# Optimization experiments

Hardware: AMD Instinct MI355X
Metric: run time of the kernel (lower is better)

The kernel has to match this reference:

```python
import jax, jax.numpy as jnp
import numpy as np

B, L, G, HID, H, D = 2, 4096, 256, 768, 12, 64
R = 127            # local_radius
BLK = R + 1        # block_len = 128
N = L // BLK       # 32 blocks (L divisible by BLK)
W = 2 * R + 1      # 255 local window
V = 32             # relative vocab size


def setup_inputs() -> dict:
    ks = jax.random.split(jax.random.key(0), 40)
    inp = {}
    inp["long_input"] = jax.random.normal(ks[0], (B, L, HID), jnp.float32)
    inp["global_input"] = jax.random.normal(ks[1], (B, G, HID), jnp.float32)
    inp["l2l_att_mask"] = jax.random.randint(ks[2], (B, L, W), 0, 2, jnp.int32)
    inp["g2g_att_mask"] = jax.random.randint(ks[3], (B, G, G), 0, 2, jnp.int32)
    inp["l2g_att_mask"] = jax.random.randint(ks[4], (B, L, G), 0, 2, jnp.int32)
    inp["g2l_att_mask"] = jax.random.randint(ks[5], (B, G, L), 0, 2, jnp.int32)
    inp["l2l_relative_att_ids"] = jax.random.randint(ks[6], (B, L, W), 0, V, jnp.int32)
    inp["g2g_relative_att_ids"] = jax.random.randint(ks[7], (B, G, G), 0, V, jnp.int32)
    inp["l2g_relative_att_ids"] = jax.random.randint(ks[8], (B, L, G), 0, V, jnp.int32)
    inp["g2l_relative_att_ids"] = jax.random.randint(ks[9], (B, G, L), 0, V, jnp.int32)
    i = 10
    for nm in ["q_long", "k_long", "v_long", "q_glob", "k_glob", "v_glob"]:
        inp["w" + nm] = 0.02 * jax.random.normal(ks[i], (HID, H * D), jnp.float32); i += 1
        inp["b" + nm] = jnp.zeros((H * D,), jnp.float32)
    inp["rel_emb_long"] = 0.5 * jax.random.normal(ks[i], (V, H, D), jnp.float32); i += 1
    inp["rel_bias_long"] = jnp.zeros((V, H), jnp.float32)
    inp["rel_emb_glob"] = 0.5 * jax.random.normal(ks[i], (V, H, D), jnp.float32); i += 1
    inp["rel_bias_glob"] = jnp.zeros((V, H), jnp.float32)
    inp["wo_long"] = 0.02 * jax.random.normal(ks[i], (H * D, HID), jnp.float32); i += 1
    inp["bo_long"] = jnp.zeros((HID,), jnp.float32)
    inp["wo_glob"] = 0.02 * jax.random.normal(ks[i], (H * D, HID), jnp.float32); i += 1
    inp["bo_glob"] = jnp.zeros((HID,), jnp.float32)
    return inp


def _expand_local(x):
    """[B, L, W] local-window ids -> blocked [B, N, BLK, 3*BLK] (skew + pad),
    zeroing entries outside the local window or outside the sequence."""
    xb = x.reshape(B, N, BLK, W)
    p = jnp.arange(BLK)[:, None]        # query pos within block
    c = jnp.arange(3 * BLK)[None, :]    # key pos within 3-block window
    r = c - p - 1                       # index into the 2R+1 window
    valid = (r >= 0) & (r < W)
    rc = jnp.clip(r, 0, W - 1)
    out = jnp.take_along_axis(xb, jnp.broadcast_to(rc, (B, N, BLK, 3 * BLK)), axis=-1)
    j = (jnp.arange(N)[:, None, None] - 1) * BLK + c  # absolute key position
    valid_full = valid[None] & (j >= 0) & (j < L)     # [N, BLK, 3*BLK]
    return out * valid_full[None].astype(x.dtype)


def reference(long_input, global_input,
              l2l_att_mask, g2g_att_mask, l2g_att_mask, g2l_att_mask,
              l2l_relative_att_ids, g2g_relative_att_ids,
              l2g_relative_att_ids, g2l_relative_att_ids,
              wq_long, bq_long, wk_long, bk_long, wv_long, bv_long,
              wq_glob, bq_glob, wk_glob, bk_glob, wv_glob, bv_glob,
              rel_emb_long, rel_bias_long, rel_emb_glob, rel_bias_glob,
              wo_long, bo_long, wo_glob, bo_glob):
    scale = 1.0 / jnp.sqrt(jnp.float32(D))

    def proj(x, w, b):
        return (x @ w + b).reshape(x.shape[0], x.shape[1], H, D)

    lq, lk, lv = proj(long_input, wq_long, bq_long), proj(long_input, wk_long, bk_long), proj(long_input, wv_long, bv_long)
    gq, gk, gv = proj(global_input, wq_glob, bq_glob), proj(global_input, wk_glob, bk_glob), proj(global_input, wv_glob, bv_glob)

    # ---- long tokens: blocked local attention fused with side (global) keys ----
    qb = lq.reshape(B, N, BLK, H, D)

    def concat3(x):
        xb = x.reshape(B, N, BLK, H, D)
        pad = jnp.zeros_like(xb[:, :1])
        xp = jnp.concatenate([pad, xb, pad], axis=1)  # [B, N+2, BLK, H, D]
        return jnp.concatenate([xp[:, :-2], xp[:, 1:-1], xp[:, 2:]], axis=2)  # [B,N,3BLK,H,D]

    keys = jnp.concatenate([concat3(lk), jnp.broadcast_to(gk[:, None], (B, N, G, H, D))], axis=2)
    vals = jnp.concatenate([concat3(lv), jnp.broadcast_to(gv[:, None], (B, N, G, H, D))], axis=2)

    mask = jnp.concatenate([_expand_local(l2l_att_mask), l2g_att_mask.reshape(B, N, BLK, G)], axis=-1)
    ids = jnp.concatenate([_expand_local(l2l_relative_att_ids), l2g_relative_att_ids.reshape(B, N, BLK, G)], axis=-1)

    scores = jnp.einsum('bnqhd,bnkhd->bnqkh', qb, keys)
    rel_all = jnp.einsum('bnqhd,rhd->bnqrh', qb, rel_emb_long) + rel_bias_long
    rel = jnp.take_along_axis(rel_all, jnp.broadcast_to(ids[..., None], ids.shape + (H,)), axis=3)
    scores = (scores + rel) * scale
    scores = scores - 10000.0 * (1.0 - mask[..., None].astype(scores.dtype))
    probs = jax.nn.softmax(scores, axis=3)
    long_ctx = jnp.einsum('bnqkh,bnkhd->bnqhd', probs, vals).reshape(B, L, H * D)
    long_out = long_ctx @ wo_long + bo_long

    # ---- global tokens: full attention over [global; long] keys ----
    kf = jnp.concatenate([gk, lk], axis=1)
    vf = jnp.concatenate([gv, lv], axis=1)
    gmask = jnp.concatenate([g2g_att_mask, g2l_att_mask], axis=-1)
    gids = jnp.concatenate([g2g_relative_att_ids, g2l_relative_att_ids], axis=-1)
    gs = jnp.einsum('bqhd,bkhd->bqkh', gq, kf)
    grel_all = jnp.einsum('bqhd,rhd->bqrh', gq, rel_emb_glob) + rel_bias_glob
    grel = jnp.take_along_axis(grel_all, jnp.broadcast_to(gids[..., None], gids.shape + (H,)), axis=2)
    gs = (gs + grel) * scale
    gs = gs - 10000.0 * (1.0 - gmask[..., None].astype(gs.dtype))
    gp = jax.nn.softmax(gs, axis=2)
    glob_ctx = jnp.einsum('bqkh,bkhd->bqhd', gp, vf).reshape(B, G, H * D)
    glob_out = glob_ctx @ wo_glob + bo_glob

    return long_out, glob_out
```

## Files before the change

kernel.cpp:

```cpp
#include <hip/hip_runtime.h>
#include <hip/hip_bf16.h>

typedef unsigned short u16;
typedef unsigned char u8;
typedef __attribute__((ext_vector_type(8))) short bf16x8;
typedef __attribute__((ext_vector_type(4))) float f32x4;

#define BB 2
#define LL 4096
#define GG 256
#define HH 12
#define DD 64
#define NB 32
#define WW 255
#define VV 32
#define NCHUNK 17
#define LKEY 640
#define GKEY 4352
#define WMAT 589824

__device__ __forceinline__ float bf2f(u16 u) {
  return __uint_as_float(((unsigned)u) << 16);
}
__device__ __forceinline__ u16 f2bf(float f) {
  unsigned u = __float_as_uint(f);
  u += 0x7FFFu + ((u >> 16) & 1u);
  return (u16)(u >> 16);
}
__device__ __forceinline__ float4 ld4bf(const u16* p) {
  ushort4 q = *reinterpret_cast<const ushort4*>(p);
  return make_float4(bf2f(q.x), bf2f(q.y), bf2f(q.z), bf2f(q.w));
}
__device__ __forceinline__ float ldx1(const void* p, size_t idx, bool f32m) {
  if (f32m) return reinterpret_cast<const float*>(p)[idx];
  return bf2f(reinterpret_cast<const u16*>(p)[idx]);
}
__device__ __forceinline__ void gload16(const u16* src, u16* ldsdst) {
  __builtin_amdgcn_global_load_lds(
      (const __attribute__((address_space(1))) unsigned int*)src,
      (__attribute__((address_space(3))) unsigned int*)ldsdst, 16, 0, 0);
}

__global__ void detect_dtype(const void* __restrict__ x, int* __restrict__ flag) {
  __shared__ int cnt;
  if (threadIdx.x == 0) cnt = 0;
  __syncthreads();
  const u16* p = reinterpret_cast<const u16*>(x);
  int c = 0;
  for (int i = threadIdx.x; i < 4096; i += 256) {
    int e = (p[i] >> 7) & 0xFF;
    if (e >= 134) c++;
  }
  atomicAdd(&cnt, c);
  __syncthreads();
  if (threadIdx.x == 0) *flag = (cnt >= 64) ? 1 : 0;
}

__global__ __launch_bounds__(256)
void pack_l(const int* __restrict__ m_l2l, const int* __restrict__ m_l2g,
            const int* __restrict__ i_l2l, const int* __restrict__ i_l2g,
            u8* __restrict__ pk) {
  const unsigned idx = blockIdx.x * 256u + threadIdx.x;
  const unsigned c = idx % (unsigned)LKEY;
  const unsigned bt = idx / (unsigned)LKEY;
  const int t = bt & (LL - 1);
  int mask = 0, id = 0;
  if (c < 384u) {
    const int rr = (int)c - (t & 127) - 1;
    const int jabs = (((t >> 7) - 1) << 7) + (int)c;
    if (rr >= 0 && rr < WW && jabs >= 0 && jabs < LL) {
      const size_t base = (size_t)bt * WW + rr;
      mask = m_l2l[base]; id = i_l2l[base];
    }
  } else {
    const size_t base = (size_t)bt * GG + (c - 384u);
    mask = m_l2g[base]; id = i_l2g[base];
  }
  pk[idx] = (u8)((id & 31) | ((mask ^ 1) << 7));
}

__global__ __launch_bounds__(256)
void pack_g(const int* __restrict__ m_g2g, const int* __restrict__ m_g2l,
            const int* __restrict__ i_g2g, const int* __restrict__ i_g2l,
            u8* __restrict__ pk) {
  const unsigned idx = blockIdx.x * 256u + threadIdx.x;
  const unsigned c = idx % (unsigned)GKEY;
  const unsigned bq = idx / (unsigned)GKEY;
  int mask, id;
  if (c < 256u) {
    const size_t base = (size_t)bq * GG + c;
    mask = m_g2g[base]; id = i_g2g[base];
  } else {
    const size_t base = (size_t)bq * (size_t)LL + (c - 256u);
    mask = m_g2l[base]; id = i_g2l[base];
  }
  pk[idx] = (u8)((id & 31) | ((mask ^ 1) << 7));
}

__global__ __launch_bounds__(256)
void wprep(const void* __restrict__ W0, const void* __restrict__ W1,
           const void* __restrict__ W2, const void* __restrict__ W3,
           const void* __restrict__ W4, const void* __restrict__ W5,
           u16* __restrict__ wt, const int* __restrict__ flagp) {
  const bool f32m = (*flagp != 0);
  const int mat = blockIdx.z;
  const void* Wm = (mat == 0) ? W0 : (mat == 1) ? W1 : (mat == 2) ? W2
                   : (mat == 3) ? W3 : (mat == 4) ? W4 : W5;
  const int n0 = blockIdx.x << 6, k0 = blockIdx.y << 6;
  const int tid = threadIdx.x;
  __shared__ u16 T[64][72];
  {
    const int r = tid >> 2, c0 = (tid & 3) << 4;
    if (f32m) {
      const float* wp = reinterpret_cast<const float*>(Wm) + (size_t)(k0 + r) * 768 + n0 + c0;
      #pragma unroll
      for (int j = 0; j < 16; j += 4) {
        float4 v = *reinterpret_cast<const float4*>(wp + j);
        T[r][c0 + j + 0] = f2bf(v.x); T[r][c0 + j + 1] = f2bf(v.y);
        T[r][c0 + j + 2] = f2bf(v.z); T[r][c0 + j + 3] = f2bf(v.w);
      }
    } else {
      const u16* wp = reinterpret_cast<const u16*>(Wm) + (size_t)(k0 + r) * 768 + n0 + c0;
      *reinterpret_cast<int4*>(&T[r][c0]) = reinterpret_cast<const int4*>(wp)[0];
      *reinterpret_cast<int4*>(&T[r][c0 + 8]) = reinterpret_cast<const int4*>(wp)[1];
    }
  }
  __syncthreads();
  {
    const int n = tid >> 2, kc0 = (tid & 3) << 4;
    u16 buf[16];
    #pragma unroll
    for (int j = 0; j < 16; j++) buf[j] = T[kc0 + j][n];
    u16* op = wt + ((size_t)mat * WMAT) + (size_t)(n0 + n) * 768 + k0 + kc0;
    *reinterpret_cast<int4*>(op) = *reinterpret_cast<int4*>(buf);
    *reinterpret_cast<int4*>(op + 8) = *reinterpret_cast<int4*>(buf + 8);
  }
}

__global__ __launch_bounds__(256)
void xprep(const void* __restrict__ x, u16* __restrict__ out,
           const int* __restrict__ flagp) {
  const bool f32m = (*flagp != 0);
  const size_t i = ((size_t)blockIdx.x * 256 + threadIdx.x) << 3;
  if (f32m) {
    const float* p = reinterpret_cast<const float*>(x) + i;
    float4 a = *reinterpret_cast<const float4*>(p);
    float4 b = *reinterpret_cast<const float4*>(p + 4);
    u16 o[8] = {f2bf(a.x), f2bf(a.y), f2bf(a.z), f2bf(a.w),
                f2bf(b.x), f2bf(b.y), f2bf(b.z), f2bf(b.w)};
    *reinterpret_cast<int4*>(out + i) = *reinterpret_cast<int4*>(o);
  } else {
    *reinterpret_cast<int4*>(out + i) =
        *reinterpret_cast<const int4*>(reinterpret_cast<const u16*>(x) + i);
  }
}

#define GEMM_CORE(A_, Wt_, row0_, ncol0_)                                        \
  __shared__ u16 lds[16384];                                                     \
  const int tid = threadIdx.x;                                                   \
  const int w = tid >> 6, l = tid & 63;                                          \
  const int lm = l & 15, quad = l >> 4;                                          \
  const int wr = w >> 1, wc = w & 1;                                             \
  const int rb = (w << 5) + (l >> 3);                                            \
  const int c8 = (l & 7) ^ (l >> 3);                                             \
  const u16* asrc = A_ + (size_t)(row0_ + rb) * 768 + (c8 << 3);                 \
  const u16* bsrc = Wt_ + (size_t)(ncol0_ + rb) * 768 + (c8 << 3);               \
  u16* adst = lds + (w << 11) + (l << 3);                                        \
  u16* bdst = adst + 8192;                                                       \
  f32x4 acc[4][4];                                                               \
  _Pragma("unroll")                                                              \
  for (int mt = 0; mt < 4; mt++)                                                 \
    _Pragma("unroll")                                                            \
    for (int nt = 0; nt < 4; nt++) acc[mt][nt] = (f32x4){0.f, 0.f, 0.f, 0.f};    \
  const char* abase = reinterpret_cast<const char*>(lds);                        \
  const char* bbase = abase + 16384;                                             \
  const int xorv = (lm & 7) << 4;                                                \
  for (int k0 = 0; k0 < 768; k0 += 64) {                                         \
    __syncthreads();                                                             \
    _Pragma("unroll")                                                            \
    for (int i = 0; i < 4; i++) gload16(asrc + k0 + i * 6144, adst + (i << 9));  \
    _Pragma("unroll")                                                            \
    for (int i = 0; i < 4; i++) gload16(bsrc + k0 + i * 6144, bdst + (i << 9));  \
    __syncthreads();                                                             \
    _Pragma("unroll")                                                            \
    for (int kk = 0; kk < 2; kk++) {                                             \
      bf16x8 af[4], bfr[4];                                                      \
      _Pragma("unroll")                                                          \
      for (int mt = 0; mt < 4; mt++)                                             \
        af[mt] = *reinterpret_cast<const bf16x8*>(                               \
            abase + ((wr << 6) + (mt << 4) + lm) * 128 +                         \
            (((kk << 6) + (quad << 4)) ^ xorv));                                 \
      _Pragma("unroll")                                                          \
      for (int nt = 0; nt < 4; nt++)                                             \
        bfr[nt] = *reinterpret_cast<const bf16x8*>(                              \
            bbase + ((wc << 6) + (nt << 4) + lm) * 128 +                         \
            (((kk << 6) + (quad << 4)) ^ xorv));                                 \
      _Pragma("unroll")                                                          \
      for (int mt = 0; mt < 4; mt++)                                             \
        _Pragma("unroll")                                                        \
        for (int nt = 0; nt < 4; nt++)                                           \
          acc[mt][nt] = __builtin_amdgcn_mfma_f32_16x16x32_bf16(                 \
              af[mt], bfr[nt], acc[mt][nt], 0, 0, 0);                            \
    }                                                                            \
  }

__global__ __launch_bounds__(256)
void gemm_qkv(const u16* __restrict__ A, const u16* __restrict__ Wt,
              const void* __restrict__ b0, const void* __restrict__ b1,
              const void* __restrict__ b2,
              u16* __restrict__ C0, u16* __restrict__ C1, u16* __restrict__ C2,
              const int* __restrict__ flagp) {
  const bool f32m = (*flagp != 0);
  int lx = blockIdx.x, ly = blockIdx.y;
  if (gridDim.y == 64) {
    const int fid = blockIdx.x + gridDim.x * blockIdx.y;
    const int x = fid & 7, r = fid >> 3;
    ly = (x << 3) | (r & 7);
    lx = r >> 3;
  }
  const int row0 = ly << 7;
  const int ncol0 = lx << 7;
  GEMM_CORE(A, Wt, row0, ncol0)

  const int which = lx / 6;
  const void* bias = (which == 0) ? b0 : ((which == 1) ? b1 : b2);
  u16* Cv = (which == 0) ? C0 : ((which == 1) ? C1 : C2);
  const float sc = (which == 0) ? 0.125f : 1.0f;
  const int colw = (lx % 6) << 7;
  #pragma unroll
  for (int nt = 0; nt < 4; nt++) {
    const int gcol = colw + (wc << 6) + (nt << 4) + lm;
    const float bv = ldx1(bias, gcol, f32m);
    #pragma unroll
    for (int mt = 0; mt < 4; mt++)
      #pragma unroll
      for (int r = 0; r < 4; r++) {
        const int grow = row0 + (wr << 6) + (mt << 4) + (quad << 2) + r;
        Cv[(size_t)grow * 768 + gcol] = f2bf((acc[mt][nt][r] + bv) * sc);
      }
  }
}

__global__ __launch_bounds__(256)
void gemm_out(const u16* __restrict__ A, const u16* __restrict__ Wt,
              const void* __restrict__ bias, void* __restrict__ Cv,
              size_t c_off, const int* __restrict__ flagp) {
  const bool f32m = (*flagp != 0);
  int lx = blockIdx.x, ly = blockIdx.y;
  if (gridDim.y == 64) {
    const int fid = blockIdx.x + gridDim.x * blockIdx.y;
    const int x = fid & 7, r = fid >> 3;
    ly = (x << 3) | (r & 7);
    lx = r >> 3;
  }
  const int row0 = ly << 7;
  const int ncol0 = lx << 7;
  GEMM_CORE(A, Wt, row0, ncol0)

  #pragma unroll
  for (int nt = 0; nt < 4; nt++) {
    const int gcol = ncol0 + (wc << 6) + (nt << 4) + lm;
    const float bv = ldx1(bias, gcol, f32m);
    #pragma unroll
    for (int mt = 0; mt < 4; mt++)
      #pragma unroll
      for (int r = 0; r < 4; r++) {
        const int grow = row0 + (wr << 6) + (mt << 4) + (quad << 2) + r;
        const float v = acc[mt][nt][r] + bv;
        if (f32m)
          reinterpret_cast<float*>(Cv)[c_off + (size_t)grow * 768 + gcol] = v;
        else
          reinterpret_cast<u16*>(Cv)[c_off + (size_t)grow * 768 + gcol] = f2bf(v);
      }
  }
}

__global__ __launch_bounds__(256)
void relk(const u16* __restrict__ Q, const void* __restrict__ emb,
          const void* __restrict__ bias, u16* __restrict__ outp, int T,
          const int* __restrict__ flagp) {
  const bool f32m = (*flagp != 0);
  const int h = blockIdx.y, b = blockIdx.z;
  const int t0 = blockIdx.x << 6;
  const int tid = threadIdx.x;
  __shared__ float Qst[64][68];
  __shared__ float Es[64][36];
  #pragma unroll
  for (int i = 0; i < 4; i++) {
    const int idx = tid + (i << 8);
    const int tt = idx >> 4, d = (idx & 15) << 2;
    float4 v = ld4bf(Q + (((size_t)b * T + t0 + tt) * HH + h) * DD + d);
    Qst[d + 0][tt] = v.x; Qst[d + 1][tt] = v.y;
    Qst[d + 2][tt] = v.z; Qst[d + 3][tt] = v.w;
  }
  #pragma unroll
  for (int i = 0; i < 8; i++) {
    const int idx = tid + (i << 8);
    const int r = idx >> 6, d = idx & 63;
    Es[d][r] = ldx1(emb, ((size_t)r * HH + h) * DD + d, f32m);
  }
  __syncthreads();
  const int tq = (tid & 31) << 1;
  const int r0 = (tid >> 5) << 2;
  float acc[2][4] = {};
  #pragma unroll 8
  for (int d = 0; d < 64; d++) {
    float2 qq = *reinterpret_cast<const float2*>(&Qst[d][tq]);
    float4 e = *reinterpret_cast<const float4*>(&Es[d][r0]);
    acc[0][0] += qq.x * e.x; acc[0][1] += qq.x * e.y;
    acc[0][2] += qq.x * e.z; acc[0][3] += qq.x * e.w;
    acc[1][0] += qq.y * e.x; acc[1][1] += qq.y * e.y;
    acc[1][2] += qq.y * e.z; acc[1][3] += qq.y * e.w;
  }
  float bv[4];
  #pragma unroll
  for (int j = 0; j < 4; j++) bv[j] = ldx1(bias, (size_t)(r0 + j) * HH + h, f32m) * 0.125f;
  #pragma unroll
  for (int i = 0; i < 2; i++) {
    ushort4 o;
    o.x = f2bf(acc[i][0] + bv[0]); o.y = f2bf(acc[i][1] + bv[1]);
    o.z = f2bf(acc[i][2] + bv[2]); o.w = f2bf(acc[i][3] + bv[3]);
    *reinterpret_cast<ushort4*>(&outp[(((size_t)b * T + t0 + tq + i) * HH + h) * VV + r0]) = o;
  }
}

__global__ __launch_bounds__(512)
void lattn(const u16* __restrict__ lq, const u16* __restrict__ lk, const u16* __restrict__ lv,
           const u16* __restrict__ gk, const u16* __restrict__ gv,
           const u8* __restrict__ pkl, const u16* __restrict__ rel,
           u16* __restrict__ lctx) {
  const int fid = blockIdx.x + 12 * (blockIdx.y + (blockIdx.z << 5));
  const int hg = fid >> 3;
  const int h = hg % 12;
  const int fl = (fid & 7) + ((hg / 12) << 3);
  const int n = fl & 31, b = fl >> 5;
  const int tid = threadIdx.x;
  __shared__ u16 Kt[64][72];
  __shared__ u16 Vt[64][74];
  __shared__ u16 Pt[128][74];
  __shared__ u16 Rl[128][36];

  const int lane = tid & 63, wv = tid >> 6;
  const int ln = lane & 15, quad = lane >> 4;
  const int tbase = n << 7;

  {
    const int qr = (wv << 4) + (lane >> 2);
    const int seg = (lane & 3) << 3;
    *reinterpret_cast<int4*>(&Rl[qr][seg]) = *reinterpret_cast<const int4*>(
        rel + (((size_t)b * LL + tbase + qr) * HH + h) * VV + seg);
  }

  bf16x8 aq[2];
  {
    const int t = tbase + (wv << 4) + ln;
    const u16* qp = lq + (((size_t)b * LL + t) * HH + h) * DD + (quad << 3);
    aq[0] = *reinterpret_cast<const bf16x8*>(qp);
    aq[1] = *reinterpret_cast<const bf16x8*>(qp + 32);
  }

  const u8* pkb = pkl + ((size_t)b * LL + tbase) * LKEY;
  const int skey = tid >> 3, sdg = (tid & 7) << 3;

  f32x4 Oacc[4];
  #pragma unroll
  for (int dt = 0; dt < 4; dt++) Oacc[dt] = (f32x4){0.f, 0.f, 0.f, 0.f};
  float lpart[4] = {};

  for (int tile = 0; tile < 10; tile++) {
    const int c0 = tile << 6;
    const bool isg = (tile >= 6);

    float badd[16];
    #pragma unroll
    for (int r = 0; r < 4; r++) {
      const int qrow = (wv << 4) + (quad << 2) + r;
      const u8* prow = pkb + qrow * LKEY + c0 + ln;
      #pragma unroll
      for (int kt = 0; kt < 4; kt++) {
        const u8 pb = prow[kt << 4];
        const float rv = bf2f(Rl[qrow][pb & 31]);
        badd[(kt << 2) + r] = (pb & 0x80) ? (rv - 10000.f) : rv;
      }
    }

    __syncthreads();
    {
      int4 kraw = {0, 0, 0, 0}, vraw = {0, 0, 0, 0};
      if (isg) {
        const size_t base = (((size_t)b * GG + (c0 - 384) + skey) * HH + h) * DD + sdg;
        kraw = *reinterpret_cast<const int4*>(gk + base);
        vraw = *reinterpret_cast<const int4*>(gv + base);
      } else {
        const int jabs = ((n - 1) << 7) + c0 + skey;
        if (jabs >= 0 && jabs < LL) {
          const size_t base = (((size_t)b * LL + jabs) * HH + h) * DD + sdg;
          kraw = *reinterpret_cast<const int4*>(lk + base);
          vraw = *reinterpret_cast<const int4*>(lv + base);
        }
      }
      *reinterpret_cast<int4*>(&Kt[skey][sdg]) = kraw;
      u16 vb[8];
      *reinterpret_cast<int4*>(vb) = vraw;
      #pragma unroll
      for (int j = 0; j < 8; j++) Vt[sdg + j][skey] = vb[j];
    }
    __syncthreads();

    f32x4 Sacc[4];
    #pragma unroll
    for (int kt = 0; kt < 4; kt++) Sacc[kt] = (f32x4){0.f, 0.f, 0.f, 0.f};
    __builtin_amdgcn_s_setprio(1);
    #pragma unroll
    for (int kk = 0; kk < 2; kk++) {
      bf16x8 bk[4];
      #pragma unroll
      for (int kt = 0; kt < 4; kt++)
        bk[kt] = *reinterpret_cast<const bf16x8*>(&Kt[(kt << 4) + ln][(kk << 5) + (quad << 3)]);
      #pragma unroll
      for (int kt = 0; kt < 4; kt++)
        Sacc[kt] = __builtin_amdgcn_mfma_f32_16x16x32_bf16(aq[kk], bk[kt], Sacc[kt], 0, 0, 0);
    }
    __builtin_amdgcn_s_setprio(0);

    #pragma unroll
    for (int kt = 0; kt < 4; kt++)
      #pragma unroll
      for (int r = 0; r < 4; r++) {
        const int ql = (wv << 4) + (quad << 2) + r;
        float s = fminf(fmaxf(Sacc[kt][r], -60.f), 60.f) + badd[(kt << 2) + r];
        const u16 p16 = f2bf(__expf(s));
        Pt[ql][(kt << 4) + ln] = p16;
        lpart[r] += bf2f(p16);
      }

    __builtin_amdgcn_s_setprio(1);
    #pragma unroll
    for (int kk = 0; kk < 2; kk++) {
      bf16x8 ap = *reinterpret_cast<const bf16x8*>(&Pt[(wv << 4) + ln][(kk << 5) + (quad << 3)]);
      #pragma unroll
      for (int dt = 0; dt < 4; dt++) {
        bf16x8 bv = *reinterpret_cast<const bf16x8*>(&Vt[(dt << 4) + ln][(kk << 5) + (quad << 3)]);
        Oacc[dt] = __builtin_amdgcn_mfma_f32_16x16x32_bf16(ap, bv, Oacc[dt], 0, 0, 0);
      }
    }
    __builtin_amdgcn_s_setprio(0);
  }

  #pragma unroll
  for (int r = 0; r < 4; r++) {
    float v = lpart[r];
    v += __shfl_xor(v, 1); v += __shfl_xor(v, 2);
    v += __shfl_xor(v, 4); v += __shfl_xor(v, 8);
    const float inv = 1.0f / v;
    const int t = tbase + (wv << 4) + (quad << 2) + r;
    const size_t base = (((size_t)b * LL + t) * HH + h) * DD;
    #pragma unroll
    for (int dt = 0; dt < 4; dt++)
      lctx[base + (dt << 4) + ln] = f2bf(Oacc[dt][r] * inv);
  }
}

__global__ __launch_bounds__(256)
void gattn(const u16* __restrict__ gq, const u16* __restrict__ gk, const u16* __restrict__ gv,
           const u16* __restrict__ lk, const u16* __restrict__ lv,
           const u8* __restrict__ pkg, const u16* __restrict__ relg,
           float* __restrict__ po, float* __restrict__ pl) {
  const int fid = blockIdx.x + 12 * (blockIdx.y + 17 * blockIdx.z);
  const int hg = fid >> 3;
  const int h = hg % 12;
  const int fl = (fid & 7) + ((hg / 12) << 3);
  const int chunk = fl % 17;
  const int bqt = fl / 17;
  const int b = bqt >> 2, qt = bqt & 3;
  const int tid = threadIdx.x;
  __shared__ u16 Kt[64][72];
  __shared__ u16 Vt[64][74];
  __shared__ u16 Pt[64][74];
  __shared__ u16 Rg[64][36];

  const int lane = tid & 63, wv = tid >> 6;
  const int ln = lane & 15, quad = lane >> 4;
  const int kbase = chunk << 8;
  const bool isgg = (chunk == 0);

  {
    const int qr = (wv << 4) + (lane >> 2);
    const int seg = (lane & 3) << 3;
    *reinterpret_cast<int4*>(&Rg[qr][seg]) = *reinterpret_cast<const int4*>(
        relg + (((size_t)b * GG + (qt << 6) + qr) * HH + h) * VV + seg);
  }

  bf16x8 aq[2];
  {
    const int qa = (qt << 6) + (wv << 4) + ln;
    const u16* qp = gq + (((size_t)b * GG + qa) * HH + h) * DD + (quad << 3);
    aq[0] = *reinterpret_cast<const bf16x8*>(qp);
    aq[1] = *reinterpret_cast<const bf16x8*>(qp + 32);
  }

  const u8* pkb = pkg + ((size_t)b * GG + (qt << 6)) * GKEY;

  f32x4 Oacc[4];
  #pragma unroll
  for (int dt = 0; dt < 4; dt++) Oacc[dt] = (f32x4){0.f, 0.f, 0.f, 0.f};
  float lpart[4] = {};

  for (int tile = 0; tile < 4; tile++) {
    const int c0 = kbase + (tile << 6);

    float badd[16];
    #pragma unroll
    for (int r = 0; r < 4; r++) {
      const int qrow = (wv << 4) + (quad << 2) + r;
      const u8* prow = pkb + qrow * GKEY + c0 + ln;
      #pragma unroll
      for (int kt = 0; kt < 4; kt++) {
        const u8 pb = prow[kt << 4];
        const float rv = bf2f(Rg[qrow][pb & 31]);
        badd[(kt << 2) + r] = (pb & 0x80) ? (rv - 10000.f) : rv;
      }
    }

    __syncthreads();
    #pragma unroll
    for (int p = 0; p < 2; p++) {
      const int idx = tid + (p << 8);
      const int key = idx >> 3, dg = (idx & 7) << 3;
      const int kc = c0 + key;
      int4 kraw, vraw;
      if (isgg) {
        const size_t base = (((size_t)b * GG + kc) * HH + h) * DD + dg;
        kraw = *reinterpret_cast<const int4*>(gk + base);
        vraw = *reinterpret_cast<const int4*>(gv + base);
      } else {
        const size_t base = (((size_t)b * LL + (kc - 256)) * HH + h) * DD + dg;
        kraw = *reinterpret_cast<const int4*>(lk + base);
        vraw = *reinterpret_cast<const int4*>(lv + base);
      }
      *reinterpret_cast<int4*>(&Kt[key][dg]) = kraw;
      u16 vb[8];
      *reinterpret_cast<int4*>(vb) = vraw;
      #pragma unroll
      for (int j = 0; j < 8; j++) Vt[dg + j][key] = vb[j];
    }
    __syncthreads();

    f32x4 Sacc[4];
    #pragma unroll
    for (int kt = 0; kt < 4; kt++) Sacc[kt] = (f32x4){0.f, 0.f, 0.f, 0.f};
    __builtin_amdgcn_s_setprio(1);
    #pragma unroll
    for (int kk = 0; kk < 2; kk++) {
      bf16x8 bk[4];
      #pragma unroll
      for (int kt = 0; kt < 4; kt++)
        bk[kt] = *reinterpret_cast<const bf16x8*>(&Kt[(kt << 4) + ln][(kk << 5) + (quad << 3)]);
      #pragma unroll
      for (int kt = 0; kt < 4; kt++)
        Sacc[kt] = __builtin_amdgcn_mfma_f32_16x16x32_bf16(aq[kk], bk[kt], Sacc[kt], 0, 0, 0);
    }
    __builtin_amdgcn_s_setprio(0);

    #pragma unroll
    for (int kt = 0; kt < 4; kt++)
      #pragma unroll
      for (int r = 0; r < 4; r++) {
        const int ql = (wv << 4) + (quad << 2) + r;
        float s = fminf(fmaxf(Sacc[kt][r], -60.f), 60.f) + badd[(kt << 2) + r];
        const u16 p16 = f2bf(__expf(s));
        Pt[ql][(kt << 4) + ln] = p16;
        lpart[r] += bf2f(p16);
      }

    __builtin_amdgcn_s_setprio(1);
    #pragma unroll
    for (int kk = 0; kk < 2; kk++) {
      bf16x8 ap = *reinterpret_cast<const bf16x8*>(&Pt[(wv << 4) + ln][(kk << 5) + (quad << 3)]);
      #pragma unroll
      for (int dt = 0; dt < 4; dt++) {
        bf16x8 bv = *reinterpret_cast<const bf16x8*>(&Vt[(dt << 4) + ln][(kk << 5) + (quad << 3)]);
        Oacc[dt] = __builtin_amdgcn_mfma_f32_16x16x32_bf16(ap, bv, Oacc[dt], 0, 0, 0);
      }
    }
    __builtin_amdgcn_s_setprio(0);
  }

  #pragma unroll
  for (int r = 0; r < 4; r++) {
    float v = lpart[r];
    v += __shfl_xor(v, 1); v += __shfl_xor(v, 2);
    v += __shfl_xor(v, 4); v += __shfl_xor(v, 8);
    const int qa = (qt << 6) + (wv << 4) + (quad << 2) + r;
    if (ln == 0)
      pl[(((size_t)chunk * BB + b) * HH + h) * GG + qa] = v;
    const size_t base = ((((size_t)chunk * BB + b) * HH + h) * GG + qa) * DD;
    #pragma unroll
    for (int dt = 0; dt < 4; dt++)
      po[base + (dt << 4) + ln] = Oacc[dt][r];
  }
}

__global__ __launch_bounds__(256)
void gcombine(const float* __restrict__ po, const float* __restrict__ pl,
              u16* __restrict__ gctx) {
  const int flat = blockIdx.x * 256 + threadIdx.x;
  const int d = flat & 63;
  const int rest = flat >> 6;
  const int h = rest % HH;
  const int bq = rest / HH;
  const int b = bq >> 8, qg = bq & 255;
  float so = 0.f, sl = 0.f;
  #pragma unroll
  for (int c = 0; c < NCHUNK; c++) {
    so += po[((((size_t)c * BB + b) * HH + h) * GG + qg) * DD + d];
    sl += pl[(((size_t)c * BB + b) * HH + h) * GG + qg];
  }
  gctx[flat] = f2bf(so / sl);
}

extern "C" void kernel_launch(void* const* d_in, const int* in_sizes, int n_in,
                              void* d_out, int out_size, void* d_ws, size_t ws_size,
                              hipStream_t stream) {
  (void)in_sizes; (void)n_in; (void)out_size; (void)ws_size;
  const void* x_long = d_in[0];
  const void* x_glob = d_in[1];
  const int* m_l2l = (const int*)d_in[2];
  const int* m_g2g = (const int*)d_in[3];
  const int* m_l2g = (const int*)d_in[4];
  const int* m_g2l = (const int*)d_in[5];
  const int* i_l2l = (const int*)d_in[6];
  const int* i_g2g = (const int*)d_in[7];
  const int* i_l2g = (const int*)d_in[8];
  const int* i_g2l = (const int*)d_in[9];
  const void* wq_l = d_in[10]; const void* bq_l = d_in[11];
  const void* wk_l = d_in[12]; const void* bk_l = d_in[13];
  const void* wv_l = d_in[14]; const void* bv_l = d_in[15];
  const void* wq_g = d_in[16]; const void* bq_g = d_in[17];
  const void* wk_g = d_in[18]; const void* bk_g = d_in[19];
  const void* wv_g = d_in[20]; const void* bv_g = d_in[21];
  const void* rel_emb_l = d_in[22]; const void* rel_bias_l = d_in[23];
  const void* rel_emb_g = d_in[24]; const void* rel_bias_g = d_in[25];
  const void* wo_l = d_in[26]; const void* bo_l = d_in[27];
  const void* wo_g = d_in[28]; const void* bo_g = d_in[29];

  constexpr size_t NLQ = (size_t)BB * LL * HH * DD;
  constexpr size_t NG  = (size_t)BB * GG * HH * DD;
  constexpr size_t NRL = (size_t)BB * LL * HH * VV;
  constexpr size_t NRG = (size_t)BB * GG * HH * VV;
  u16* lqw  = reinterpret_cast<u16*>(d_ws);
  u16* lkw  = lqw + NLQ;
  u16* lvw  = lkw + NLQ;
  u16* gqw  = lvw + NLQ;
  u16* gkw  = gqw + NG;
  u16* gvw  = gkw + NG;
  u16* rell = gvw + NG;
  u16* relg = rell + NRL;
  u16* lctx = relg + NRG;
  u16* gctx = lctx + NLQ;
  int* flag = reinterpret_cast<int*>(gctx + NG);
  float* po = reinterpret_cast<float*>(flag + 16);
  float* pl = po + (size_t)NCHUNK * BB * HH * GG * DD;
  u8* pk_l = reinterpret_cast<u8*>(po);
  u16* wt_qkv = reinterpret_cast<u16*>(po) + 2621440;
  u16* xl_bf = lctx;
  u16* xg_bf = gctx;
  u8* pk_g = reinterpret_cast<u8*>(pl + (size_t)NCHUNK * BB * HH * GG);
  u16* wt_o = reinterpret_cast<u16*>(pk_g + (size_t)BB * GG * GKEY);

  dim3 t256(256);
  detect_dtype<<<1, t256, 0, stream>>>(x_long, flag);
  pack_l<<<dim3((BB * LL * LKEY) / 256), t256, 0, stream>>>(m_l2l, m_l2g, i_l2l, i_l2g, pk_l);
  pack_g<<<dim3((BB * GG * GKEY) / 256), t256, 0, stream>>>(m_g2g, m_g2l, i_g2g, i_g2l, pk_g);
  wprep<<<dim3(12, 12, 6), t256, 0, stream>>>(wq_l, wk_l, wv_l, wq_g, wk_g, wv_g, wt_qkv, flag);
  wprep<<<dim3(12, 12, 2), t256, 0, stream>>>(wo_l, wo_g, wo_l, wo_l, wo_l, wo_l, wt_o, flag);
  xprep<<<dim3((BB * LL * 768) / 2048), t256, 0, stream>>>(x_long, xl_bf, flag);
  xprep<<<dim3((BB * GG * 768) / 2048), t256, 0, stream>>>(x_glob, xg_bf, flag);
  gemm_qkv<<<dim3(18, 64), t256, 0, stream>>>(xl_bf, wt_qkv, bq_l, bk_l, bv_l,
                                              lqw, lkw, lvw, flag);
  gemm_qkv<<<dim3(18, 4), t256, 0, stream>>>(xg_bf, wt_qkv + (size_t)3 * WMAT,
                                             bq_g, bk_g, bv_g, gqw, gkw, gvw, flag);
  relk<<<dim3(64, 12, 2), t256, 0, stream>>>(lqw, rel_emb_l, rel_bias_l, rell, LL, flag);
  relk<<<dim3(4, 12, 2), t256, 0, stream>>>(gqw, rel_emb_g, rel_bias_g, relg, GG, flag);
  lattn<<<dim3(12, 32, 2), dim3(512), 0, stream>>>(lqw, lkw, lvw, gkw, gvw,
                                                   pk_l, rell, lctx);
  gattn<<<dim3(12, NCHUNK, 8), t256, 0, stream>>>(gqw, gkw, gvw, lkw, lvw,
                                                  pk_g, relg, po, pl);
  gcombine<<<dim3(1536), t256, 0, stream>>>(po, pl, gctx);
  gemm_out<<<dim3(6, 64), t256, 0, stream>>>(lctx, wt_o, bo_l, d_out, 0, flag);
  gemm_out<<<dim3(6, 4), t256, 0, stream>>>(gctx, wt_o + WMAT, bo_g, d_out,
                                            (size_t)BB * LL * 768, flag);
}
```

Baseline: 437.0 us.

## Prefetch next K/V tile and mask bytes into registers during attention loops

```diff
diff --git a/kernel.cpp b/kernel.cpp
--- a/kernel.cpp
+++ b/kernel.cpp
@@ -362,48 +362,71 @@
   const u8* pkb = pkl + ((size_t)b * LL + tbase) * LKEY;
   const int skey = tid >> 3, sdg = (tid & 7) << 3;
 
+  int4 kraw = {0, 0, 0, 0}, vraw = {0, 0, 0, 0};
+  {
+    const int jabs = ((n - 1) << 7) + skey;
+    if (jabs >= 0 && jabs < LL) {
+      const size_t base = (((size_t)b * LL + jabs) * HH + h) * DD + sdg;
+      kraw = *reinterpret_cast<const int4*>(lk + base);
+      vraw = *reinterpret_cast<const int4*>(lv + base);
+    }
+  }
+  u8 pbv[16];
+  #pragma unroll
+  for (int r = 0; r < 4; r++) {
+    const u8* prow = pkb + ((wv << 4) + (quad << 2) + r) * LKEY + ln;
+    #pragma unroll
+    for (int kt = 0; kt < 4; kt++) pbv[(kt << 2) + r] = prow[kt << 4];
+  }
+
   f32x4 Oacc[4];
   #pragma unroll
   for (int dt = 0; dt < 4; dt++) Oacc[dt] = (f32x4){0.f, 0.f, 0.f, 0.f};
   float lpart[4] = {};
 
   for (int tile = 0; tile < 10; tile++) {
-    const int c0 = tile << 6;
-    const bool isg = (tile >= 6);
-
     float badd[16];
     #pragma unroll
     for (int r = 0; r < 4; r++) {
       const int qrow = (wv << 4) + (quad << 2) + r;
-      const u8* prow = pkb + qrow * LKEY + c0 + ln;
       #pragma unroll
       for (int kt = 0; kt < 4; kt++) {
-        const u8 pb = prow[kt << 4];
+        const u8 pb = pbv[(kt << 2) + r];
         const float rv = bf2f(Rl[qrow][pb & 31]);
         badd[(kt << 2) + r] = (pb & 0x80) ? (rv - 10000.f) : rv;
       }
     }
 
     __syncthreads();
+    *reinterpret_cast<int4*>(&Kt[skey][sdg]) = kraw;
     {
-      int4 kraw = {0, 0, 0, 0}, vraw = {0, 0, 0, 0};
-      if (isg) {
-        const size_t base = (((size_t)b * GG + (c0 - 384) + skey) * HH + h) * DD + sdg;
-        kraw = *reinterpret_cast<const int4*>(gk + base);
-        vraw = *reinterpret_cast<const int4*>(gv + base);
+      u16 vb[8];
+      *reinterpret_cast<int4*>(vb) = vraw;
+      #pragma unroll
+      for (int j = 0; j < 8; j++) Vt[sdg + j][skey] = vb[j];
+    }
+    if (tile < 9) {
+      const int c1 = (tile + 1) << 6;
+      int4 k2 = {0, 0, 0, 0}, v2 = {0, 0, 0, 0};
+      if (tile + 1 >= 6) {
+        const size_t base = (((size_t)b * GG + (c1 - 384) + skey) * HH + h) * DD + sdg;
+        k2 = *reinterpret_cast<const int4*>(gk + base);
+        v2 = *reinterpret_cast<const int4*>(gv + base);
       } else {
-        const int jabs = ((n - 1) << 7) + c0 + skey;
+        const int jabs = ((n - 1) << 7) + c1 + skey;
         if (jabs >= 0 && jabs < LL) {
           const size_t base = (((size_t)b * LL + jabs) * HH + h) * DD + sdg;
-          kraw = *reinterpret_cast<const int4*>(lk + base);
-          vraw = *reinterpret_cast<const int4*>(lv + base);
+          k2 = *reinterpret_cast<const int4*>(lk + base);
+          v2 = *reinterpret_cast<const int4*>(lv + base);
         }
       }
-      *reinterpret_cast<int4*>(&Kt[skey][sdg]) = kraw;
-      u16 vb[8];
-      *reinterpret_cast<int4*>(vb) = vraw;
-      #pragma unroll
-      for (int j = 0; j < 8; j++) Vt[sdg + j][skey] = vb[j];
+      kraw = k2; vraw = v2;
+      #pragma unroll
+      for (int r = 0; r < 4; r++) {
+        const u8* prow = pkb + ((wv << 4) + (quad << 2) + r) * LKEY + c1 + ln;
+        #pragma unroll
+        for (int kt = 0; kt < 4; kt++) pbv[(kt << 2) + r] = prow[kt << 4];
+      }
     }
     __syncthreads();
 
@@ -428,7 +451,7 @@
       #pragma unroll
       for (int r = 0; r < 4; r++) {
         const int ql = (wv << 4) + (quad << 2) + r;
-        float s = fminf(fmaxf(Sacc[kt][r], -60.f), 60.f) + badd[(kt << 2) + r];
+        const float s = Sacc[kt][r] + badd[(kt << 2) + r];
         const u16 p16 = f2bf(__expf(s));
         Pt[ql][(kt << 4) + ln] = p16;
         lpart[r] += bf2f(p16);
@@ -500,6 +523,29 @@
   }
 
   const u8* pkb = pkg + ((size_t)b * GG + (qt << 6)) * GKEY;
+  const int skey = tid >> 3, sdg = (tid & 7) << 3;
+
+  int4 kraw[2], vraw[2];
+  #pragma unroll
+  for (int p = 0; p < 2; p++) {
+    const int kc = kbase + skey + (p << 5);
+    if (isgg) {
+      const size_t base = (((size_t)b * GG + kc) * HH + h) * DD + sdg;
+      kraw[p] = *reinterpret_cast<const int4*>(gk + base);
+      vraw[p] = *reinterpret_cast<const int4*>(gv + base);
+    } else {
+      const size_t base = (((size_t)b * LL + (kc - 256)) * HH + h) * DD + sdg;
+      kraw[p] = *reinterpret_cast<const int4*>(lk + base);
+      vraw[p] = *reinterpret_cast<const int4*>(lv + base);
+    }
+  }
+  u8 pbv[16];
+  #pragma unroll
+  for (int r = 0; r < 4; r++) {
+    const u8* prow = pkb + ((wv << 4) + (quad << 2) + r) * GKEY + kbase + ln;
+    #pragma unroll
+    for (int kt = 0; kt < 4; kt++) pbv[(kt << 2) + r] = prow[kt << 4];
+  }
 
   f32x4 Oacc[4];
   #pragma unroll
@@ -507,16 +553,13 @@
   float lpart[4] = {};
 
   for (int tile = 0; tile < 4; tile++) {
-    const int c0 = kbase + (tile << 6);
-
     float badd[16];
     #pragma unroll
     for (int r = 0; r < 4; r++) {
       const int qrow = (wv << 4) + (quad << 2) + r;
-      const u8* prow = pkb + qrow * GKEY + c0 + ln;
       #pragma unroll
       for (int kt = 0; kt < 4; kt++) {
-        const u8 pb = prow[kt << 4];
+        const u8 pb = pbv[(kt << 2) + r];
         const float rv = bf2f(Rg[qrow][pb & 31]);
         badd[(kt << 2) + r] = (pb & 0x80) ? (rv - 10000.f) : rv;
       }
@@ -525,24 +568,34 @@
     __syncthreads();
     #pragma unroll
     for (int p = 0; p < 2; p++) {
-      const int idx = tid + (p << 8);
-      const int key = idx >> 3, dg = (idx & 7) << 3;
-      const int kc = c0 + key;
-      int4 kraw, vraw;
-      if (isgg) {
-        const size_t base = (((size_t)b * GG + kc) * HH + h) * DD + dg;
-        kraw = *reinterpret_cast<const int4*>(gk + base);
-        vraw = *reinterpret_cast<const int4*>(gv + base);
-      } else {
-        const size_t base = (((size_t)b * LL + (kc - 256)) * HH + h) * DD + dg;
-        kraw = *reinterpret_cast<const int4*>(lk + base);
-        vraw = *reinterpret_cast<const int4*>(lv + base);
-      }
-      *reinterpret_cast<int4*>(&Kt[key][dg]) = kraw;
+      const int key = skey + (p << 5);
+      *reinterpret_cast<int4*>(&Kt[key][sdg]) = kraw[p];
       u16 vb[8];
-      *reinterpret_cast<int4*>(vb) = vraw;
-      #pragma unroll
-      for (int j = 0; j < 8; j++) Vt[dg + j][key] = vb[j];
+      *reinterpret_cast<int4*>(vb) = vraw[p];
+      #pragma unroll
+      for (int j = 0; j < 8; j++) Vt[sdg + j][key] = vb[j];
+    }
+    if (tile < 3) {
+      const int c1 = kbase + ((tile + 1) << 6);
+      #pragma unroll
+      for (int p = 0; p < 2; p++) {
+        const int kc = c1 + skey + (p << 5);
+        if (isgg) {
+          const size_t base = (((size_t)b * GG + kc) * HH + h) * DD + sdg;
+          kraw[p] = *reinterpret_cast<const int4*>(gk + base);
+          vraw[p] = *reinterpret_cast<const int4*>(gv + base);
+        } else {
+          const size_t base = (((size_t)b * LL + (kc - 256)) * HH + h) * DD + sdg;
+          kraw[p] = *reinterpret_cast<const int4*>(lk + base);
+          vraw[p] = *reinterpret_cast<const int4*>(lv + base);
+        }
+      }
+      #pragma unroll
+      for (int r = 0; r < 4; r++) {
+        const u8* prow = pkb + ((wv << 4) + (quad << 2) + r) * GKEY + c1 + ln;
+        #pragma unroll
+        for (int kt = 0; kt < 4; kt++) pbv[(kt << 2) + r] = prow[kt << 4];
+      }
     }
     __syncthreads();
 
@@ -567,7 +620,7 @@
       #pragma unroll
       for (int r = 0; r < 4; r++) {
         const int ql = (wv << 4) + (quad << 2) + r;
-        float s = fminf(fmaxf(Sacc[kt][r], -60.f), 60.f) + badd[(kt << 2) + r];
+        const float s = Sacc[kt][r] + badd[(kt << 2) + r];
         const u16 p16 = f2bf(__expf(s));
         Pt[ql][(kt << 4) + ln] = p16;
         lpart[r] += bf2f(p16);
```

Result: no change. 434.8 us (-0.5%).

## Reorder packed local mask layout and interleave P/V columns for vectorized access

Applied to the files above, without the earlier changes.

```diff
diff --git a/kernel.cpp b/kernel.cpp
--- a/kernel.cpp
+++ b/kernel.cpp
@@ -3,6 +3,7 @@
 
 typedef unsigned short u16;
 typedef unsigned char u8;
+typedef unsigned int u32;
 typedef __attribute__((ext_vector_type(8))) short bf16x8;
 typedef __attribute__((ext_vector_type(4))) float f32x4;
 
@@ -61,19 +62,25 @@
             const int* __restrict__ i_l2l, const int* __restrict__ i_l2g,
             u8* __restrict__ pk) {
   const unsigned idx = blockIdx.x * 256u + threadIdx.x;
-  const unsigned c = idx % (unsigned)LKEY;
-  const unsigned bt = idx / (unsigned)LKEY;
-  const int t = bt & (LL - 1);
+  const int pos = idx & 63;
+  const int lnp = pos >> 2, ktp = pos & 3;
+  const int qrow = (idx >> 6) & 127;
+  const unsigned rest = idx >> 13;
+  const int tile = rest % 10;
+  const unsigned bn = rest / 10;
+  const int n = bn & 31, b = bn >> 5;
+  const int c = (tile << 6) + (ktp << 4) + lnp;
+  const unsigned bt = (unsigned)b * LL + (n << 7) + qrow;
   int mask = 0, id = 0;
-  if (c < 384u) {
-    const int rr = (int)c - (t & 127) - 1;
-    const int jabs = (((t >> 7) - 1) << 7) + (int)c;
+  if (c < 384) {
+    const int rr = c - qrow - 1;
+    const int jabs = ((n - 1) << 7) + c;
     if (rr >= 0 && rr < WW && jabs >= 0 && jabs < LL) {
       const size_t base = (size_t)bt * WW + rr;
       mask = m_l2l[base]; id = i_l2l[base];
     }
   } else {
-    const size_t base = (size_t)bt * GG + (c - 384u);
+    const size_t base = (size_t)bt * GG + (c - 384);
     mask = m_l2g[base]; id = i_l2g[base];
   }
   pk[idx] = (u8)((id & 31) | ((mask ^ 1) << 7));
@@ -327,7 +334,7 @@
 __global__ __launch_bounds__(512)
 void lattn(const u16* __restrict__ lq, const u16* __restrict__ lk, const u16* __restrict__ lv,
            const u16* __restrict__ gk, const u16* __restrict__ gv,
-           const u8* __restrict__ pkl, const u16* __restrict__ rel,
+           const u32* __restrict__ pkl, const u16* __restrict__ rel,
            u16* __restrict__ lctx) {
   const int fid = blockIdx.x + 12 * (blockIdx.y + (blockIdx.z << 5));
   const int hg = fid >> 3;
@@ -337,7 +344,7 @@
   const int tid = threadIdx.x;
   __shared__ u16 Kt[64][72];
   __shared__ u16 Vt[64][74];
-  __shared__ u16 Pt[128][74];
+  __shared__ u16 Pt[128][76];
   __shared__ u16 Rl[128][36];
 
   const int lane = tid & 63, wv = tid >> 6;
@@ -359,8 +366,9 @@
     aq[1] = *reinterpret_cast<const bf16x8*>(qp + 32);
   }
 
-  const u8* pkb = pkl + ((size_t)b * LL + tbase) * LKEY;
+  const u32* pk32 = pkl + (size_t)(b * 32 + n) * 20480;
   const int skey = tid >> 3, sdg = (tid & 7) << 3;
+  const int scol = ((skey & 15) << 2) | (skey >> 4);
 
   f32x4 Oacc[4];
   #pragma unroll
@@ -375,12 +383,12 @@
     #pragma unroll
     for (int r = 0; r < 4; r++) {
       const int qrow = (wv << 4) + (quad << 2) + r;
-      const u8* prow = pkb + qrow * LKEY + c0 + ln;
+      const u32 pw = pk32[(((tile << 7) + qrow) << 4) + ln];
       #pragma unroll
       for (int kt = 0; kt < 4; kt++) {
-        const u8 pb = prow[kt << 4];
+        const u32 pb = (pw >> (kt << 3)) & 0xFFu;
         const float rv = bf2f(Rl[qrow][pb & 31]);
-        badd[(kt << 2) + r] = (pb & 0x80) ? (rv - 10000.f) : rv;
+        badd[(kt << 2) + r] = (pb & 0x80u) ? (rv - 10000.f) : rv;
       }
     }
 
@@ -403,7 +411,7 @@
       u16 vb[8];
       *reinterpret_cast<int4*>(vb) = vraw;
       #pragma unroll
-      for (int j = 0; j < 8; j++) Vt[sdg + j][skey] = vb[j];
+      for (int j = 0; j < 8; j++) Vt[sdg + j][scol] = vb[j];
     }
     __syncthreads();
 
@@ -424,15 +432,20 @@
     __builtin_amdgcn_s_setprio(0);
 
     #pragma unroll
-    for (int kt = 0; kt < 4; kt++)
-      #pragma unroll
-      for (int r = 0; r < 4; r++) {
-        const int ql = (wv << 4) + (quad << 2) + r;
-        float s = fminf(fmaxf(Sacc[kt][r], -60.f), 60.f) + badd[(kt << 2) + r];
-        const u16 p16 = f2bf(__expf(s));
-        Pt[ql][(kt << 4) + ln] = p16;
-        lpart[r] += bf2f(p16);
-      }
+    for (int r = 0; r < 4; r++) {
+      const int ql = (wv << 4) + (quad << 2) + r;
+      const float p0 = __expf(Sacc[0][r] + badd[0 + r]);
+      const float p1 = __expf(Sacc[1][r] + badd[4 + r]);
+      const float p2 = __expf(Sacc[2][r] + badd[8 + r]);
+      const float p3 = __expf(Sacc[3][r] + badd[12 + r]);
+      u32 w0, w1;
+      asm("v_cvt_pk_bf16_f32 %0, %1, %2" : "=v"(w0) : "v"(p0), "v"(p1));
+      asm("v_cvt_pk_bf16_f32 %0, %1, %2" : "=v"(w1) : "v"(p2), "v"(p3));
+      uint2 wp; wp.x = w0; wp.y = w1;
+      *reinterpret_cast<uint2*>(&Pt[ql][ln << 2]) = wp;
+      lpart[r] += __uint_as_float(w0 << 16) + __uint_as_float(w0 & 0xFFFF0000u)
+                + __uint_as_float(w1 << 16) + __uint_as_float(w1 & 0xFFFF0000u);
+    }
 
     __builtin_amdgcn_s_setprio(1);
     #pragma unroll
@@ -567,7 +580,7 @@
       #pragma unroll
       for (int r = 0; r < 4; r++) {
         const int ql = (wv << 4) + (quad << 2) + r;
-        float s = fminf(fmaxf(Sacc[kt][r], -60.f), 60.f) + badd[(kt << 2) + r];
+        const float s = Sacc[kt][r] + badd[(kt << 2) + r];
         const u16 p16 = f2bf(__expf(s));
         Pt[ql][(kt << 4) + ln] = p16;
         lpart[r] += bf2f(p16);
@@ -683,7 +696,7 @@
   relk<<<dim3(64, 12, 2), t256, 0, stream>>>(lqw, rel_emb_l, rel_bias_l, rell, LL, flag);
   relk<<<dim3(4, 12, 2), t256, 0, stream>>>(gqw, rel_emb_g, rel_bias_g, relg, GG, flag);
   lattn<<<dim3(12, 32, 2), dim3(512), 0, stream>>>(lqw, lkw, lvw, gkw, gvw,
-                                                   pk_l, rell, lctx);
+                                                   reinterpret_cast<const u32*>(pk_l), rell, lctx);
   gattn<<<dim3(12, NCHUNK, 8), t256, 0, stream>>>(gqw, gkw, gvw, lkw, lvw,
                                                   pk_g, relg, po, pl);
   gcombine<<<dim3(1536), t256, 0, stream>>>(po, pl, gctx);
```

Result: no change. 428.8 us (-1.9%).
